# Kernel optimization log

Hardware: AMD Instinct MI355X
Metric: run time of the kernel (lower is better)

The kernel has to match this reference:

```python
import jax, jax.numpy as jnp
import numpy as np

B, N, HL, D, HID, O, E, S, K = 8, 64, 32, 256, 1024, 256, 8, 3, 2


def setup_inputs() -> dict:
    key = jax.random.key(0)
    ks = jax.random.split(key, 12)
    w = 0.02
    return {
        "feature_vectors": jax.random.normal(ks[0], (B, N, HL, D), dtype=jnp.float32),
        "object_types": jax.random.uniform(ks[1], (B, N, HL, S, 1), dtype=jnp.float32),
        "gate_w": jax.random.normal(ks[2], (D, E), dtype=jnp.float32) * w,
        "gate_b": jnp.zeros((E,), dtype=jnp.float32),
        "shared_w1": jax.random.normal(ks[3], (S, D, HID), dtype=jnp.float32) * w,
        "shared_b1": jnp.zeros((S, HID), dtype=jnp.float32),
        "shared_w2": jax.random.normal(ks[4], (S, HID, O), dtype=jnp.float32) * w,
        "shared_b2": jnp.zeros((S, O), dtype=jnp.float32),
        "ind_w1": jax.random.normal(ks[5], (E, D, HID), dtype=jnp.float32) * w,
        "ind_b1": jnp.zeros((E, HID), dtype=jnp.float32),
        "ind_w2": jax.random.normal(ks[6], (E, HID, O), dtype=jnp.float32) * w,
        "ind_b2": jnp.zeros((E, O), dtype=jnp.float32),
    }


def reference(feature_vectors, object_types, gate_w, gate_b,
              shared_w1, shared_b1, shared_w2, shared_b2,
              ind_w1, ind_b1, ind_w2, ind_b2):
    b, n, hl, d = feature_vectors.shape
    x = feature_vectors.reshape(-1, d)                      # (T, D)
    T = x.shape[0]

    # gating: softmax -> top-k -> renormalize selected probs
    gates = jax.nn.softmax(x @ gate_w + gate_b, axis=-1)    # (T, E)
    vals, idx = jax.lax.top_k(gates, K)                     # (T, K)
    w = vals / vals.sum(axis=-1, keepdims=True)
    # dense (T, E) combine weights: zero outside top-k, equivalent to scatter-add loop
    w_full = jnp.zeros_like(gates).at[jnp.arange(T)[:, None], idx].set(w)

    # shared experts: all S experts on every token, weighted by object_types
    sh_h = jax.nn.relu(jnp.einsum('td,sdh->tsh', x, shared_w1) + shared_b1)
    sh_o = jnp.einsum('tsh,sho->tso', sh_h, shared_w2) + shared_b2  # (T, S, O)
    obj = object_types.reshape(-1, S, 1)                    # (T, S, 1)
    shared_out = (sh_o * obj).sum(axis=1)                   # (T, O)

    # independent experts: dense all-expert GEMM, combined by masked gate weights
    ih = jax.nn.relu(jnp.einsum('td,edh->teh', x, ind_w1) + ind_b1)
    io = jnp.einsum('teh,eho->teo', ih, ind_w2) + ind_b2    # (T, E, O)
    ind_out = jnp.einsum('te,teo->to', w_full, io)          # (T, O)

    out = 0.5 * shared_out + 0.5 * ind_out
    return out.reshape(b, n, hl, -1)
```

## Files before the change

### kernel.cpp

```cpp
#include <hip/hip_runtime.h>
#include <hip/hip_bf16.h>
#include <stdint.h>

#define TOK   16384
#define DIM   256
#define HIDN  1024
#define OUTD  256
#define NEXP  8
#define NSH   3
#define NSLOT 11
#define TM    64
#define NCH   32
#define HSTR  40

typedef short bf16x8  __attribute__((ext_vector_type(8)));
typedef float f32x4   __attribute__((ext_vector_type(4)));
typedef short short4v __attribute__((ext_vector_type(4)));

constexpr size_t XB_OFF   = 0;
constexpr size_t W1P_OFF  = XB_OFF  + (size_t)TOK*DIM*2;
constexpr size_t W2P_OFF  = W1P_OFF + (size_t)NSLOT*DIM*HIDN*2;
constexpr size_t WTS_OFF  = W2P_OFF + (size_t)NSLOT*HIDN*OUTD*2;
constexpr size_t IDS_OFF  = WTS_OFF + (size_t)TOK*2*4;
constexpr size_t CNT_OFF  = IDS_OFF + (size_t)TOK*2*4;
constexpr size_t LTOK_OFF = CNT_OFF + 256;
constexpr size_t LW_OFF   = LTOK_OFF + (size_t)NEXP*TOK*4;
constexpr size_t WS_NEED  = LW_OFF + (size_t)NEXP*TOK*4;

__device__ __forceinline__ unsigned short f2bf(float f) {
    __hip_bfloat16 h = __float2bfloat16(f);
    return *reinterpret_cast<unsigned short*>(&h);
}

__device__ __forceinline__ f32x4 mfma16(bf16x8 a, bf16x8 b, f32x4 c) {
    return __builtin_amdgcn_mfma_f32_16x16x32_bf16(a, b, c, 0, 0, 0);
}

__device__ __forceinline__ void gload_lds16(const void* g, void* l) {
    __builtin_amdgcn_global_load_lds(
        (const __attribute__((address_space(1))) unsigned int*)g,
        (__attribute__((address_space(3))) unsigned int*)l, 16, 0, 0);
}

__device__ __forceinline__ void fence_sched() { __builtin_amdgcn_sched_barrier(0); }

__global__ __launch_bounds__(256) void k_prep(
    const float* __restrict__ x, const float* __restrict__ gw,
    const float* __restrict__ gb, short* __restrict__ xb,
    float* __restrict__ wts, int* __restrict__ ids) {
    int wid = threadIdx.x >> 6, lane = threadIdx.x & 63;
    int t = blockIdx.x * 4 + wid;
    const float* xr = x + (size_t)t * DIM;
    {
        float4 v = reinterpret_cast<const float4*>(xr)[lane];
        short4v o;
        o[0] = (short)f2bf(v.x); o[1] = (short)f2bf(v.y);
        o[2] = (short)f2bf(v.z); o[3] = (short)f2bf(v.w);
        reinterpret_cast<short4v*>(xb + (size_t)t * DIM)[lane] = o;
    }
    float acc[NEXP] = {0.f,0.f,0.f,0.f,0.f,0.f,0.f,0.f};
    #pragma unroll
    for (int i = 0; i < DIM/64; ++i) {
        int d = i*64 + lane;
        float xv = xr[d];
        const float* g = gw + (size_t)d * NEXP;
        #pragma unroll
        for (int e = 0; e < NEXP; ++e) acc[e] = fmaf(xv, g[e], acc[e]);
    }
    #pragma unroll
    for (int off = 32; off; off >>= 1) {
        #pragma unroll
        for (int e = 0; e < NEXP; ++e) acc[e] += __shfl_xor(acc[e], off, 64);
    }
    if (lane == 0) {
        float l[NEXP];
        #pragma unroll
        for (int e = 0; e < NEXP; ++e) l[e] = acc[e] + gb[e];
        int e0 = 0; float v0 = l[0];
        #pragma unroll
        for (int e = 1; e < NEXP; ++e) if (l[e] > v0) { v0 = l[e]; e0 = e; }
        int e1 = -1; float v1 = -1e30f;
        #pragma unroll
        for (int e = 0; e < NEXP; ++e) if (e != e0 && l[e] > v1) { v1 = l[e]; e1 = e; }
        float r = expf(v1 - v0);
        float w0 = 0.5f / (1.f + r);
        float w1 = 0.5f * r / (1.f + r);
        ids[2*t]   = e0;  ids[2*t+1] = e1;
        wts[2*t]   = w0;  wts[2*t+1] = w1;
    }
}

__global__ __launch_bounds__(256) void k_convert_w(
    const float* __restrict__ sw1, const float* __restrict__ iw1,
    const float* __restrict__ sw2, const float* __restrict__ iw2,
    short* __restrict__ w1p, short* __restrict__ w2p) {
    __shared__ float tile[32][68];
    int bid = blockIdx.x, tid = threadIdx.x;
    const int W1B = NSLOT * 8 * 16;
    bool isW1 = bid < W1B;
    int b = isW1 ? bid : bid - W1B;
    int NTG = isW1 ? 16 : 4;
    int KT  = isW1 ? 8 : 32;
    int NT  = isW1 ? 64 : 16;
    int Nd  = isW1 ? HIDN : OUTD;
    int ntg = b % NTG; b /= NTG;
    int kt  = b % KT;
    int slot = b / KT;
    const float* src;
    if (isW1) src = (slot < NSH) ? sw1 + (size_t)slot*DIM*HIDN  : iw1 + (size_t)(slot-NSH)*DIM*HIDN;
    else      src = (slot < NSH) ? sw2 + (size_t)slot*HIDN*OUTD : iw2 + (size_t)(slot-NSH)*HIDN*OUTD;
    {
        int tr = tid >> 3, tc = (tid & 7) * 8;
        const float* s = src + (size_t)(kt*32 + tr)*Nd + ntg*64 + tc;
        float4 v0 = *reinterpret_cast<const float4*>(s);
        float4 v1 = *reinterpret_cast<const float4*>(s + 4);
        *reinterpret_cast<float4*>(&tile[tr][tc])     = v0;
        *reinterpret_cast<float4*>(&tile[tr][tc + 4]) = v1;
    }
    __syncthreads();
    {
        int ntl = tid >> 6, lane = tid & 63;
        int n  = ntl*16 + (lane & 15);
        int k8 = (lane >> 4) * 8;
        bf16x8 o;
        #pragma unroll
        for (int j = 0; j < 8; ++j) o[j] = (short)f2bf(tile[k8 + j][n]);
        size_t gidx = (((size_t)slot*KT + kt)*NT + ntg*4 + ntl)*64 + lane;
        short* dst = isW1 ? w1p : w2p;
        reinterpret_cast<bf16x8*>(dst)[gidx] = o;
    }
}

__global__ __launch_bounds__(256) void k_route(
    const int* __restrict__ ids, const float* __restrict__ wts,
    int* __restrict__ cnt, int* __restrict__ ltok, float* __restrict__ lw) {
    __shared__ int lcnt[NEXP];
    __shared__ int gbase[NEXP];
    int tid = threadIdx.x;
    if (tid < NEXP) lcnt[tid] = 0;
    __syncthreads();
    int t = blockIdx.x * 256 + tid;
    int e0 = ids[2*t], e1 = ids[2*t+1];
    int p0 = atomicAdd(&lcnt[e0], 1);
    int p1 = atomicAdd(&lcnt[e1], 1);
    __syncthreads();
    if (tid < NEXP) gbase[tid] = atomicAdd(&cnt[tid], lcnt[tid]);
    __syncthreads();
    size_t o0 = (size_t)e0*TOK + gbase[e0] + p0;
    size_t o1 = (size_t)e1*TOK + gbase[e1] + p1;
    ltok[o0] = t;  lw[o0] = wts[2*t];
    ltok[o1] = t;  lw[o1] = wts[2*t+1];
}

__global__ __launch_bounds__(512) void k_moe(
    const short* __restrict__ xb, const short* __restrict__ w1p, const short* __restrict__ w2p,
    const float* __restrict__ sb1, const float* __restrict__ sb2,
    const float* __restrict__ ib1, const float* __restrict__ ib2,
    const float* __restrict__ obj, const int* __restrict__ cnt,
    const int* __restrict__ ltok, const float* __restrict__ lw,
    float* __restrict__ out)
{
    __shared__ __align__(16) char Wb1[2][16384];
    __shared__ __align__(16) char Wb2[2][16384];
    __shared__ __align__(16) short Hs[TM * HSTR];
    __shared__ float bias_lds[HIDN];
    __shared__ int   tokl[TM];
    __shared__ float twl[TM];

    const int slot = blockIdx.y;
    const int m0   = blockIdx.x * TM;
    const bool sh  = slot < NSH;
    const int e    = slot - NSH;
    int count = TOK;
    if (!sh) { count = cnt[e]; if (m0 >= count) return; }

    const int tid  = threadIdx.x;
    const int w    = tid >> 6, lane = tid & 63;
    const int wm   = w >> 1,   wn   = w & 1;
    const int pm   = w >> 2,   pn   = w & 3;
    const int lrow = lane & 15, g   = lane >> 4;

    if (tid < TM) {
        if (sh) {
            tokl[tid] = m0 + tid;
            twl[tid]  = 0.5f * obj[(size_t)(m0 + tid)*NSH + slot];
        } else {
            int p = m0 + tid;
            bool ok = p < count;
            tokl[tid] = ok ? ltok[(size_t)e*TOK + p] : 0;
            twl[tid]  = ok ? lw[(size_t)e*TOK + p] : 0.f;
        }
    }
    __syncthreads();

    const char* w1base = (const char*)w1p;
    const char* w2base = (const char*)w2p;
    const float* b1v = sh ? (sb1 + slot*HIDN) : (ib1 + (size_t)e*HIDN);

    const int tokA = tokl[wm*16 + lrow];
    bf16x8 areg[8];
    #pragma unroll
    for (int kt = 0; kt < 8; ++kt)
        areg[kt] = *reinterpret_cast<const bf16x8*>(
            xb + (size_t)tokA*DIM + kt*32 + g*8);

    if (w < 4)
        gload_lds16((const char*)b1v + w*1024 + lane*16, (char*)bias_lds + w*1024);

    auto stage_w1 = [&](int c, int buf) {
        #pragma unroll
        for (int i = 0; i < 2; ++i)
            gload_lds16(
                w1base + ((((size_t)slot*8 + w)*64 + c*2 + i) << 10) + lane*16,
                Wb1[buf] + ((w*2 + i) << 10));
    };
    auto stage_w2 = [&](int c, int buf) {
        const char* s2 = w2base + ((((size_t)slot*32 + c)*16) << 10);
        #pragma unroll
        for (int i = 0; i < 2; ++i)
            gload_lds16(s2 + ((w*2 + i) << 10) + lane*16, Wb2[buf] + ((w*2 + i) << 10));
    };

    asm volatile("s_waitcnt vmcnt(0) lgkmcnt(0)" ::: "memory");
    __syncthreads();

    stage_w1(0, 0);
    stage_w2(0, 0);
    stage_w1(1, 1);

    f32x4 acc2[2][4] = {};
    for (int c = 0; c < NCH; ++c) {
        const int p = c & 1;
        if (c + 1 < NCH) {
            stage_w2(c + 1, p ^ 1);
            fence_sched();
            asm volatile("s_waitcnt vmcnt(4)" ::: "memory");
        } else {
            fence_sched();
            asm volatile("s_waitcnt vmcnt(0)" ::: "memory");
        }
        fence_sched();
        __builtin_amdgcn_s_barrier();
        fence_sched();

        f32x4 acc1 = {};
        #pragma unroll
        for (int kt = 0; kt < 8; ++kt) {
            bf16x8 b = *reinterpret_cast<const bf16x8*>(
                Wb1[p] + ((kt*2 + wn) << 10) + lane*16);
            acc1 = mfma16(areg[kt], b, acc1);
        }
        {
            int col = wn*16 + lrow;
            float bias = bias_lds[c*32 + col];
            #pragma unroll
            for (int r = 0; r < 4; ++r) {
                int row = wm*16 + g*4 + r;
                float v = fmaxf(acc1[r] + bias, 0.f) * twl[row];
                Hs[row*HSTR + col] = (short)f2bf(v);
            }
        }
        fence_sched();
        asm volatile("s_waitcnt lgkmcnt(0)" ::: "memory");
        fence_sched();
        __builtin_amdgcn_s_barrier();
        fence_sched();

        if (c + 2 < NCH) stage_w1(c + 2, p);
        fence_sched();

        {
            bf16x8 a2[2];
            #pragma unroll
            for (int mf = 0; mf < 2; ++mf)
                a2[mf] = *reinterpret_cast<const bf16x8*>(
                    Hs + (pm*32 + mf*16 + lrow)*HSTR + g*8);
            #pragma unroll
            for (int nf = 0; nf < 4; ++nf) {
                bf16x8 b2 = *reinterpret_cast<const bf16x8*>(
                    Wb2[p] + ((pn*4 + nf) << 10) + lane*16);
                #pragma unroll
                for (int mf = 0; mf < 2; ++mf)
                    acc2[mf][nf] = mfma16(a2[mf], b2, acc2[mf][nf]);
            }
        }
        fence_sched();
        __builtin_amdgcn_s_barrier();
        fence_sched();
    }

    {
        const float* b2 = sh ? (sb2 + slot*OUTD) : (ib2 + (size_t)e*OUTD);
        #pragma unroll
        for (int mf = 0; mf < 2; ++mf)
            #pragma unroll
            for (int nf = 0; nf < 4; ++nf) {
                int col = pn*64 + nf*16 + lrow;
                #pragma unroll
                for (int r = 0; r < 4; ++r) {
                    int row = pm*32 + mf*16 + g*4 + r;
                    if (sh || (m0 + row < count)) {
                        int t = tokl[row];
                        float v = acc2[mf][nf][r] + twl[row] * b2[col];
                        atomicAdd(&out[(size_t)t*OUTD + col], v);
                    }
                }
            }
    }
}

extern "C" void kernel_launch(void* const* d_in, const int* in_sizes, int n_in,
                              void* d_out, int out_size, void* d_ws, size_t ws_size,
                              hipStream_t stream) {
    const float* x   = (const float*)d_in[0];
    const float* obj = (const float*)d_in[1];
    const float* gw  = (const float*)d_in[2];
    const float* gb  = (const float*)d_in[3];
    const float* sw1 = (const float*)d_in[4];
    const float* sb1 = (const float*)d_in[5];
    const float* sw2 = (const float*)d_in[6];
    const float* sb2 = (const float*)d_in[7];
    const float* iw1 = (const float*)d_in[8];
    const float* ib1 = (const float*)d_in[9];
    const float* iw2 = (const float*)d_in[10];
    const float* ib2 = (const float*)d_in[11];
    float* out = (float*)d_out;
    char* ws = (char*)d_ws;
    if (ws_size < WS_NEED) return;

    short* xb   = (short*)(ws + XB_OFF);
    short* w1p  = (short*)(ws + W1P_OFF);
    short* w2p  = (short*)(ws + W2P_OFF);
    float* wts  = (float*)(ws + WTS_OFF);
    int*   ids  = (int*)  (ws + IDS_OFF);
    int*   cnt  = (int*)  (ws + CNT_OFF);
    int*   ltok = (int*)  (ws + LTOK_OFF);
    float* lwt  = (float*)(ws + LW_OFF);

    hipMemsetAsync(ws + CNT_OFF, 0, 256, stream);
    hipMemsetAsync(out, 0, (size_t)out_size * 4, stream);
    k_prep<<<TOK/4, 256, 0, stream>>>(x, gw, gb, xb, wts, ids);
    k_convert_w<<<NSLOT*8*16 + NSLOT*32*4, 256, 0, stream>>>(sw1, iw1, sw2, iw2, w1p, w2p);
    k_route<<<TOK/256, 256, 0, stream>>>(ids, wts, cnt, ltok, lwt);
    k_moe<<<dim3(TOK/TM, NSLOT), 512, 0, stream>>>(
        xb, w1p, w2p, sb1, sb2, ib1, ib2, obj, cnt, ltok, lwt, out);
}
```

Baseline: 203.8 us.

## Load W2 fragments directly to registers and use 32x32 MFMA for second GEMM

```diff
diff --git a/kernel.cpp b/kernel.cpp
--- a/kernel.cpp
+++ b/kernel.cpp
@@ -15,6 +15,7 @@
 
 typedef short bf16x8  __attribute__((ext_vector_type(8)));
 typedef float f32x4   __attribute__((ext_vector_type(4)));
+typedef float f32x16  __attribute__((ext_vector_type(16)));
 typedef short short4v __attribute__((ext_vector_type(4)));
 
 constexpr size_t XB_OFF   = 0;
@@ -34,6 +35,9 @@
 
 __device__ __forceinline__ f32x4 mfma16(bf16x8 a, bf16x8 b, f32x4 c) {
     return __builtin_amdgcn_mfma_f32_16x16x32_bf16(a, b, c, 0, 0, 0);
+}
+__device__ __forceinline__ f32x16 mfma32(bf16x8 a, bf16x8 b, f32x16 c) {
+    return __builtin_amdgcn_mfma_f32_32x32x16_bf16(a, b, c, 0, 0, 0);
 }
 
 __device__ __forceinline__ void gload_lds16(const void* g, void* l) {
@@ -101,7 +105,6 @@
     int b = isW1 ? bid : bid - W1B;
     int NTG = isW1 ? 16 : 4;
     int KT  = isW1 ? 8 : 32;
-    int NT  = isW1 ? 64 : 16;
     int Nd  = isW1 ? HIDN : OUTD;
     int ntg = b % NTG; b /= NTG;
     int kt  = b % KT;
@@ -118,16 +121,25 @@
         *reinterpret_cast<float4*>(&tile[tr][tc + 4]) = v1;
     }
     __syncthreads();
-    {
+    if (isW1) {
         int ntl = tid >> 6, lane = tid & 63;
         int n  = ntl*16 + (lane & 15);
         int k8 = (lane >> 4) * 8;
         bf16x8 o;
         #pragma unroll
         for (int j = 0; j < 8; ++j) o[j] = (short)f2bf(tile[k8 + j][n]);
-        size_t gidx = (((size_t)slot*KT + kt)*NT + ntg*4 + ntl)*64 + lane;
-        short* dst = isW1 ? w1p : w2p;
-        reinterpret_cast<bf16x8*>(dst)[gidx] = o;
+        size_t gidx = (((size_t)slot*8 + kt)*64 + ntg*4 + ntl)*64 + lane;
+        reinterpret_cast<bf16x8*>(w1p)[gidx] = o;
+    } else {
+        int sub = tid >> 6, lane = tid & 63;
+        int kt_sub = sub >> 1, nt_sub = sub & 1;
+        int n  = nt_sub*32 + (lane & 31);
+        int k8 = kt_sub*16 + (lane >> 5) * 8;
+        bf16x8 o;
+        #pragma unroll
+        for (int j = 0; j < 8; ++j) o[j] = (short)f2bf(tile[k8 + j][n]);
+        size_t gidx = (((size_t)slot*64 + kt*2 + kt_sub)*8 + ntg*2 + nt_sub)*64 + lane;
+        reinterpret_cast<bf16x8*>(w2p)[gidx] = o;
     }
 }
 
@@ -161,7 +173,6 @@
     float* __restrict__ out)
 {
     __shared__ __align__(16) char Wb1[2][16384];
-    __shared__ __align__(16) char Wb2[2][16384];
     __shared__ __align__(16) short Hs[TM * HSTR];
     __shared__ float bias_lds[HIDN];
     __shared__ int   tokl[TM];
@@ -177,8 +188,9 @@
     const int tid  = threadIdx.x;
     const int w    = tid >> 6, lane = tid & 63;
     const int wm   = w >> 1,   wn   = w & 1;
-    const int pm   = w >> 2,   pn   = w & 3;
+    const int pmr  = w & 1,    pnc  = w >> 1;
     const int lrow = lane & 15, g   = lane >> 4;
+    const int l31  = lane & 31, hi  = lane >> 5;
 
     if (tid < TM) {
         if (sh) {
@@ -214,31 +226,18 @@
                 w1base + ((((size_t)slot*8 + w)*64 + c*2 + i) << 10) + lane*16,
                 Wb1[buf] + ((w*2 + i) << 10));
     };
-    auto stage_w2 = [&](int c, int buf) {
-        const char* s2 = w2base + ((((size_t)slot*32 + c)*16) << 10);
-        #pragma unroll
-        for (int i = 0; i < 2; ++i)
-            gload_lds16(s2 + ((w*2 + i) << 10) + lane*16, Wb2[buf] + ((w*2 + i) << 10));
-    };
 
     asm volatile("s_waitcnt vmcnt(0) lgkmcnt(0)" ::: "memory");
     __syncthreads();
 
     stage_w1(0, 0);
-    stage_w2(0, 0);
     stage_w1(1, 1);
 
-    f32x4 acc2[2][4] = {};
+    f32x16 acc2[2] = {};
     for (int c = 0; c < NCH; ++c) {
         const int p = c & 1;
-        if (c + 1 < NCH) {
-            stage_w2(c + 1, p ^ 1);
-            fence_sched();
-            asm volatile("s_waitcnt vmcnt(4)" ::: "memory");
-        } else {
-            fence_sched();
-            asm volatile("s_waitcnt vmcnt(0)" ::: "memory");
-        }
+        if (c + 1 < NCH) { fence_sched(); asm volatile("s_waitcnt vmcnt(2)" ::: "memory"); }
+        else             { fence_sched(); asm volatile("s_waitcnt vmcnt(0)" ::: "memory"); }
         fence_sched();
         __builtin_amdgcn_s_barrier();
         fence_sched();
@@ -270,20 +269,23 @@
         fence_sched();
 
         {
-            bf16x8 a2[2];
+            bf16x8 wf[2][2];
             #pragma unroll
-            for (int mf = 0; mf < 2; ++mf)
-                a2[mf] = *reinterpret_cast<const bf16x8*>(
-                    Hs + (pm*32 + mf*16 + lrow)*HSTR + g*8);
+            for (int ks = 0; ks < 2; ++ks)
+                #pragma unroll
+                for (int j = 0; j < 2; ++j)
+                    wf[ks][j] = *reinterpret_cast<const bf16x8*>(
+                        w2base + ((((size_t)slot*64 + c*2 + ks)*8 + pnc*2 + j) << 10) + lane*16);
             #pragma unroll
-            for (int nf = 0; nf < 4; ++nf) {
-                bf16x8 b2 = *reinterpret_cast<const bf16x8*>(
-                    Wb2[p] + ((pn*4 + nf) << 10) + lane*16);
-                #pragma unroll
-                for (int mf = 0; mf < 2; ++mf)
-                    acc2[mf][nf] = mfma16(a2[mf], b2, acc2[mf][nf]);
+            for (int ks = 0; ks < 2; ++ks) {
+                bf16x8 av = *reinterpret_cast<const bf16x8*>(
+                    Hs + (pmr*32 + l31)*HSTR + ks*16 + hi*8);
+                acc2[0] = mfma32(av, wf[ks][0], acc2[0]);
+                acc2[1] = mfma32(av, wf[ks][1], acc2[1]);
             }
         }
+        fence_sched();
+        asm volatile("s_waitcnt lgkmcnt(0)" ::: "memory");
         fence_sched();
         __builtin_amdgcn_s_barrier();
         fence_sched();
@@ -292,20 +294,19 @@
     {
         const float* b2 = sh ? (sb2 + slot*OUTD) : (ib2 + (size_t)e*OUTD);
         #pragma unroll
-        for (int mf = 0; mf < 2; ++mf)
+        for (int j = 0; j < 2; ++j) {
+            int col = pnc*64 + j*32 + l31;
+            float b2v = b2[col];
             #pragma unroll
-            for (int nf = 0; nf < 4; ++nf) {
-                int col = pn*64 + nf*16 + lrow;
-                #pragma unroll
-                for (int r = 0; r < 4; ++r) {
-                    int row = pm*32 + mf*16 + g*4 + r;
-                    if (sh || (m0 + row < count)) {
-                        int t = tokl[row];
-                        float v = acc2[mf][nf][r] + twl[row] * b2[col];
-                        atomicAdd(&out[(size_t)t*OUTD + col], v);
-                    }
+            for (int r = 0; r < 16; ++r) {
+                int row = pmr*32 + (r & 3) + 8*(r >> 2) + 4*hi;
+                if (sh || (m0 + row < count)) {
+                    int t = tokl[row];
+                    float v = acc2[j][r] + twl[row] * b2v;
+                    atomicAdd(&out[(size_t)t*OUTD + col], v);
                 }
             }
+        }
     }
 }
 
```

New measurement: 217.4 us. 6.7% more time.
